# Kernel tuning notes

Measured on AMD Instinct MI355X. Metric: run time of the kernel, lower is better.

Reference implementation:

```python
import jax, jax.numpy as jnp
import numpy as np

B, N, D_MODEL = 8, 1024, 512
H, DK = 8, 64
STATIONS = 128
MASK_NEG = -1e9
LN_EPS = 1e-6


def setup_inputs() -> dict:
    key = jax.random.key(0)
    ks = jax.random.split(key, 9)
    return {
        "hidden_states": jax.random.normal(ks[0], (B, N, D_MODEL), dtype=jnp.float32),
        "rpe": jax.random.normal(ks[1], (B, H, N, N), dtype=jnp.float32) * 0.1,
        "Wq": jax.random.normal(ks[2], (H * DK, D_MODEL), dtype=jnp.float32) * 0.02,
        "Wk": jax.random.normal(ks[3], (H * DK, D_MODEL), dtype=jnp.float32) * 0.02,
        "Wv": jax.random.normal(ks[4], (H * DK, D_MODEL), dtype=jnp.float32) * 0.02,
        "fc_w": jax.random.normal(ks[5], (D_MODEL, H * DK), dtype=jnp.float32) * 0.02,
        "fc_b": jnp.zeros((D_MODEL,), dtype=jnp.float32),
        "ln_g": jnp.ones((D_MODEL,), dtype=jnp.float32),
        "ln_b": jnp.zeros((D_MODEL,), dtype=jnp.float32),
    }


def _star_mask(n, stations):
    # q_k_mask: query i attends to key j iff j < stations or i == j
    idx = jnp.arange(n)
    return (idx[None, :] < stations) | (idx[:, None] == idx[None, :])  # [n, n] bool


def reference(hidden_states, rpe, Wq, Wk, Wv, fc_w, fc_b, ln_g, ln_b):
    b, n, _ = hidden_states.shape
    residual = hidden_states
    q = (hidden_states @ Wq.T).reshape(b, n, H, DK)
    k = (hidden_states @ Wk.T).reshape(b, n, H, DK)
    v = (hidden_states @ Wv.T).reshape(b, n, H, DK)
    # sparse star+self-loop QK^T with inline RPE add (dense emulation of QKP_mm_tvm)
    scores = jnp.einsum("bihd,bjhd->bhij", q, k) + rpe  # [b,h,n,n]
    mask = _star_mask(n, STATIONS)
    scores = jnp.where(mask[None, None], scores, MASK_NEG)
    scores = scores / jnp.sqrt(jnp.float32(DK))
    attn = jax.nn.softmax(scores, axis=-1)
    # AttnV_mm_tvm: sparse attn-weights times V
    ctx = jnp.einsum("bhij,bjhd->bihd", attn, v).reshape(b, n, H * DK)
    ctx = ctx @ fc_w.T + fc_b + residual
    mu = jnp.mean(ctx, axis=-1, keepdims=True)
    var = jnp.var(ctx, axis=-1, keepdims=True)
    return (ctx - mu) / jnp.sqrt(var + LN_EPS) * ln_g + ln_b
```

## Files before the change

### kernel.cpp

```cpp
#include <hip/hip_runtime.h>
#include <hip/hip_bf16.h>
#include <math.h>

#define B_  8
#define N_  1024
#define DM  512
#define H_  8
#define DK_ 64
#define ST  128
#define QT  32

typedef __attribute__((ext_vector_type(8))) short short8;
typedef __attribute__((ext_vector_type(4))) float floatx4;

#define GLD16(gp, lp)                                                          \
    __builtin_amdgcn_global_load_lds(                                          \
        (const __attribute__((address_space(1))) void*)(gp),                   \
        (__attribute__((address_space(3))) void*)(lp), 16, 0, 0)

struct CastArgs {
    const float* src[5];
    unsigned short* dst[5];
    int n[5];
};

__global__ __launch_bounds__(256)
void cast_bf16_kernel(CastArgs a)
{
    const int j = blockIdx.y;
    const float* __restrict__ s = a.src[j];
    unsigned short* __restrict__ d = a.dst[j];
    const int n = a.n[j];
    int i = (blockIdx.x * 256 + threadIdx.x) * 8;
    if (i >= n) return;
    float4 x0 = *(const float4*)&s[i];
    float4 x1 = *(const float4*)&s[i + 4];
    ushort4 o0, o1;
    __hip_bfloat16 t;
    t = __float2bfloat16(x0.x); o0.x = *(unsigned short*)&t;
    t = __float2bfloat16(x0.y); o0.y = *(unsigned short*)&t;
    t = __float2bfloat16(x0.z); o0.z = *(unsigned short*)&t;
    t = __float2bfloat16(x0.w); o0.w = *(unsigned short*)&t;
    t = __float2bfloat16(x1.x); o1.x = *(unsigned short*)&t;
    t = __float2bfloat16(x1.y); o1.y = *(unsigned short*)&t;
    t = __float2bfloat16(x1.z); o1.z = *(unsigned short*)&t;
    t = __float2bfloat16(x1.w); o1.w = *(unsigned short*)&t;
    *(ushort4*)&d[i] = o0;
    *(ushort4*)&d[i + 4] = o1;
}

__device__ __forceinline__
void gemm_core(const unsigned short* __restrict__ A,
               const unsigned short* __restrict__ W,
               int m0, int n0, unsigned short* As, unsigned short* Bs,
               floatx4 acc[4][4])
{
    const int tid = threadIdx.x;
    const int lane = tid & 63;
    const int wave = tid >> 6;
    const int wm = wave >> 1, wn = wave & 1;
    const int srow = tid >> 2;
    const int skq  = (tid & 3) * 8;
    const unsigned short* Ag = A + (size_t)(m0 + srow) * 512 + skq;
    const unsigned short* Bg = W + (size_t)(n0 + srow) * 512 + skq;
    const int mrow = lane & 15;
    const int koff = (lane >> 4) * 8;

    for (int kt = 0; kt < 512; kt += 32) {
        __syncthreads();
        GLD16(Ag + kt,            &As[tid * 8]);
        GLD16(Ag + 64 * 512 + kt, &As[2048 + tid * 8]);
        GLD16(Bg + kt,            &Bs[tid * 8]);
        GLD16(Bg + 64 * 512 + kt, &Bs[2048 + tid * 8]);
        __syncthreads();
        short8 af[4], bf[4];
        #pragma unroll
        for (int t = 0; t < 4; ++t) {
            af[t] = *(const short8*)&As[(wm * 64 + t * 16 + mrow) * 32 + koff];
            bf[t] = *(const short8*)&Bs[(wn * 64 + t * 16 + mrow) * 32 + koff];
        }
        #pragma unroll
        for (int mt = 0; mt < 4; ++mt)
            #pragma unroll
            for (int nt = 0; nt < 4; ++nt)
                acc[mt][nt] = __builtin_amdgcn_mfma_f32_16x16x32_bf16(
                    af[mt], bf[nt], acc[mt][nt], 0, 0, 0);
    }
}

__global__ __launch_bounds__(256)
void qkv_gemm_kernel(const unsigned short* __restrict__ A,
                     const unsigned short* __restrict__ W0,
                     const unsigned short* __restrict__ W1,
                     const unsigned short* __restrict__ W2,
                     float* __restrict__ q, float* __restrict__ k,
                     float* __restrict__ v)
{
    __shared__ __align__(16) unsigned short As[128 * 32];
    __shared__ __align__(16) unsigned short Bs[128 * 32];
    const int by = blockIdx.y;
    const unsigned short* W = (by < 4) ? W0 : (by < 8 ? W1 : W2);
    float* C = (by < 4) ? q : (by < 8 ? k : v);
    const int m0 = blockIdx.x * 128;
    const int n0 = (by & 3) * 128;

    floatx4 acc[4][4];
    #pragma unroll
    for (int i = 0; i < 4; ++i)
        #pragma unroll
        for (int j = 0; j < 4; ++j)
            acc[i][j] = (floatx4){0.f, 0.f, 0.f, 0.f};

    gemm_core(A, W, m0, n0, As, Bs, acc);

    const int lane = threadIdx.x & 63;
    const int wave = threadIdx.x >> 6;
    const int wm = wave >> 1, wn = wave & 1;
    const int col = n0 + wn * 64 + (lane & 15);
    const int rq  = (lane >> 4) * 4;
    #pragma unroll
    for (int mt = 0; mt < 4; ++mt)
        #pragma unroll
        for (int nt = 0; nt < 4; ++nt)
            #pragma unroll
            for (int r = 0; r < 4; ++r)
                C[(size_t)(m0 + wm * 64 + mt * 16 + rq + r) * 512 + col + nt * 16]
                    = acc[mt][nt][r];
}

__global__ __launch_bounds__(256)
void fc_gemm_kernel(const unsigned short* __restrict__ A,
                    const unsigned short* __restrict__ W,
                    const float* __restrict__ bias,
                    const float* __restrict__ resid,
                    float* __restrict__ C)
{
    __shared__ __align__(16) unsigned short As[128 * 32];
    __shared__ __align__(16) unsigned short Bs[128 * 32];
    const int m0 = blockIdx.x * 128;
    const int n0 = blockIdx.y * 128;

    floatx4 acc[4][4];
    #pragma unroll
    for (int i = 0; i < 4; ++i)
        #pragma unroll
        for (int j = 0; j < 4; ++j)
            acc[i][j] = (floatx4){0.f, 0.f, 0.f, 0.f};

    gemm_core(A, W, m0, n0, As, Bs, acc);

    const int lane = threadIdx.x & 63;
    const int wave = threadIdx.x >> 6;
    const int wm = wave >> 1, wn = wave & 1;
    const int col = n0 + wn * 64 + (lane & 15);
    const int rq  = (lane >> 4) * 4;
    #pragma unroll
    for (int mt = 0; mt < 4; ++mt)
        #pragma unroll
        for (int nt = 0; nt < 4; ++nt) {
            const int c = col + nt * 16;
            const float b = bias[c];
            #pragma unroll
            for (int r = 0; r < 4; ++r) {
                const size_t row = (size_t)(m0 + wm * 64 + mt * 16 + rq + r);
                C[row * 512 + c] = acc[mt][nt][r] + b + resid[row * 512 + c];
            }
        }
}

__global__ __launch_bounds__(256)
void attn_kernel(const float* __restrict__ q, const float* __restrict__ k,
                 const float* __restrict__ v, const float* __restrict__ rpe,
                 unsigned short* __restrict__ ctx)
{
    __shared__ __align__(16) float Qs[64][34];
    __shared__ __align__(16) float KV[128 * 68];
    __shared__ __align__(16) float Ps[128][34];
    __shared__ float selfS[QT];

    const int tid = threadIdx.x;
    const int tx = tid & 15, ty = tid >> 4;
    const int qb = blockIdx.x * QT;
    const int h  = blockIdx.y;
    const int b  = blockIdx.z;

    const float* qg = q + (size_t)(b * N_ + qb) * DM + h * DK_;
    const float* kg = k + (size_t)b * N_ * DM + h * DK_;
    const float* vg = v + (size_t)b * N_ * DM + h * DK_;

    {
        const int row = tid >> 3;
        const int kc  = (tid & 7) << 3;
        float4 a  = *(const float4*)(qg + (size_t)row * DM + kc);
        float4 bq = *(const float4*)(qg + (size_t)row * DM + kc + 4);
        Qs[kc + 0][row] = a.x;  Qs[kc + 1][row] = a.y;
        Qs[kc + 2][row] = a.z;  Qs[kc + 3][row] = a.w;
        Qs[kc + 4][row] = bq.x; Qs[kc + 5][row] = bq.y;
        Qs[kc + 6][row] = bq.z; Qs[kc + 7][row] = bq.w;
    }
    #pragma unroll
    for (int it = 0; it < 8; ++it) {
        int id = tid + it * 256;
        int j  = id >> 4;
        int dc = (id & 15) << 2;
        float4 a = *(const float4*)(kg + (size_t)j * DM + dc);
        KV[(dc + 0) * 132 + j] = a.x;
        KV[(dc + 1) * 132 + j] = a.y;
        KV[(dc + 2) * 132 + j] = a.z;
        KV[(dc + 3) * 132 + j] = a.w;
    }
    __syncthreads();

    if (tid < QT) {
        int i = qb + tid;
        float sv = -1e30f;
        if (i >= ST) {
            float dot = 0.f;
            const float* krow = kg + (size_t)i * DM;
            for (int d = 0; d < DK_; ++d)
                dot = fmaf(Qs[d][tid], krow[d], dot);
            sv = (dot + rpe[((size_t)(b * H_ + h) * N_ + i) * N_ + i]) * 0.125f;
        }
        selfS[tid] = sv;
    }

    float s[2][8] = {};
    #pragma unroll 4
    for (int d = 0; d < 64; ++d) {
        float2 qv = *(const float2*)&Qs[d][ty << 1];
        float4 ka = *(const float4*)&KV[d * 132 + (tx << 3)];
        float4 kb = *(const float4*)&KV[d * 132 + (tx << 3) + 4];
        float kk_[8] = {ka.x, ka.y, ka.z, ka.w, kb.x, kb.y, kb.z, kb.w};
        #pragma unroll
        for (int c = 0; c < 8; ++c) {
            s[0][c] = fmaf(qv.x, kk_[c], s[0][c]);
            s[1][c] = fmaf(qv.y, kk_[c], s[1][c]);
        }
    }
    __syncthreads();

    float l_r[2], ps_r[2];
    #pragma unroll
    for (int r = 0; r < 2; ++r) {
        int i = qb + (ty << 1) + r;
        const float* rrow = rpe + ((size_t)(b * H_ + h) * N_ + i) * N_ + (tx << 3);
        float4 ra = *(const float4*)rrow;
        float4 rb = *(const float4*)(rrow + 4);
        float rr[8] = {ra.x, ra.y, ra.z, ra.w, rb.x, rb.y, rb.z, rb.w};
        float mx = -1e30f;
        #pragma unroll
        for (int c = 0; c < 8; ++c) {
            s[r][c] = (s[r][c] + rr[c]) * 0.125f;
            mx = fmaxf(mx, s[r][c]);
        }
        #pragma unroll
        for (int o = 1; o < 16; o <<= 1)
            mx = fmaxf(mx, __shfl_xor(mx, o, 64));
        float sm = selfS[(ty << 1) + r];
        mx = fmaxf(mx, sm);
        float ls = 0.f;
        float p[8];
        #pragma unroll
        for (int c = 0; c < 8; ++c) {
            p[c] = __expf(s[r][c] - mx);
            ls += p[c];
        }
        #pragma unroll
        for (int o = 1; o < 16; o <<= 1)
            ls += __shfl_xor(ls, o, 64);
        float pself = __expf(sm - mx);
        ls += pself;
        l_r[r] = ls; ps_r[r] = pself;
        #pragma unroll
        for (int c = 0; c < 8; ++c)
            Ps[(tx << 3) + c][(ty << 1) + r] = p[c];
    }
    __syncthreads();

    #pragma unroll
    for (int it = 0; it < 8; ++it) {
        int id = tid + it * 256;
        int j  = id >> 4;
        int dc = (id & 15) << 2;
        float4 a = *(const float4*)(vg + (size_t)j * DM + dc);
        *(float4*)&KV[j * 68 + dc] = a;
    }
    __syncthreads();

    float c2[2][4] = {};
    #pragma unroll 4
    for (int j = 0; j < 128; ++j) {
        float2 pv = *(const float2*)&Ps[j][ty << 1];
        float4 vv = *(const float4*)&KV[j * 68 + (tx << 2)];
        float vv_[4] = {vv.x, vv.y, vv.z, vv.w};
        #pragma unroll
        for (int c = 0; c < 4; ++c) {
            c2[0][c] = fmaf(pv.x, vv_[c], c2[0][c]);
            c2[1][c] = fmaf(pv.y, vv_[c], c2[1][c]);
        }
    }
    #pragma unroll
    for (int r = 0; r < 2; ++r) {
        int qr = (ty << 1) + r;
        int i  = qb + qr;
        if (i >= ST) {
            float4 sv4 = *(const float4*)(vg + (size_t)i * DM + (tx << 2));
            float pself = ps_r[r];
            c2[r][0] = fmaf(pself, sv4.x, c2[r][0]);
            c2[r][1] = fmaf(pself, sv4.y, c2[r][1]);
            c2[r][2] = fmaf(pself, sv4.z, c2[r][2]);
            c2[r][3] = fmaf(pself, sv4.w, c2[r][3]);
        }
        float inv = 1.0f / l_r[r];
        ushort4 o;
        __hip_bfloat16 t;
        t = __float2bfloat16(c2[r][0] * inv); o.x = *(unsigned short*)&t;
        t = __float2bfloat16(c2[r][1] * inv); o.y = *(unsigned short*)&t;
        t = __float2bfloat16(c2[r][2] * inv); o.z = *(unsigned short*)&t;
        t = __float2bfloat16(c2[r][3] * inv); o.w = *(unsigned short*)&t;
        *(ushort4*)&ctx[(size_t)(b * N_ + i) * DM + h * DK_ + (tx << 2)] = o;
    }
}

__global__ __launch_bounds__(256)
void ln_kernel(float* __restrict__ io, const float* __restrict__ g,
               const float* __restrict__ bb)
{
    const int t = blockIdx.x;
    const int tid = threadIdx.x;
    float* row = io + (size_t)t * DM;
    float2 x = *(const float2*)&row[tid * 2];
    float s  = x.x + x.y;
    float ss = fmaf(x.x, x.x, x.y * x.y);
    #pragma unroll
    for (int o = 1; o < 64; o <<= 1) {
        s  += __shfl_xor(s,  o, 64);
        ss += __shfl_xor(ss, o, 64);
    }
    __shared__ float wsum[4], wsq[4];
    const int w = tid >> 6;
    if ((tid & 63) == 0) { wsum[w] = s; wsq[w] = ss; }
    __syncthreads();
    s  = wsum[0] + wsum[1] + wsum[2] + wsum[3];
    ss = wsq[0]  + wsq[1]  + wsq[2]  + wsq[3];
    const float mean = s * (1.0f / DM);
    const float var  = ss * (1.0f / DM) - mean * mean;
    const float rstd = rsqrtf(var + 1e-6f);
    float2 gg = *(const float2*)&g[tid * 2];
    float2 bv = *(const float2*)&bb[tid * 2];
    x.x = (x.x - mean) * rstd * gg.x + bv.x;
    x.y = (x.y - mean) * rstd * gg.y + bv.y;
    *(float2*)&row[tid * 2] = x;
}

extern "C" void kernel_launch(void* const* d_in, const int* in_sizes, int n_in,
                              void* d_out, int out_size, void* d_ws, size_t ws_size,
                              hipStream_t stream)
{
    (void)in_sizes; (void)n_in; (void)out_size; (void)ws_size;
    const float* hidden = (const float*)d_in[0];
    const float* rpe    = (const float*)d_in[1];
    const float* Wq     = (const float*)d_in[2];
    const float* Wk     = (const float*)d_in[3];
    const float* Wv     = (const float*)d_in[4];
    const float* fc_w   = (const float*)d_in[5];
    const float* fc_b   = (const float*)d_in[6];
    const float* ln_g   = (const float*)d_in[7];
    const float* ln_b   = (const float*)d_in[8];
    float* out = (float*)d_out;
    char* ws = (char*)d_ws;

    const size_t MB = 1024 * 1024;
    float*          qb = (float*)(ws + 0 * MB);
    float*          kb = (float*)(ws + 16 * MB);
    float*          vb = (float*)(ws + 32 * MB);
    unsigned short* hb = (unsigned short*)(ws + 48 * MB);
    unsigned short* cb = (unsigned short*)(ws + 56 * MB);
    unsigned short* wq = (unsigned short*)(ws + 64 * MB);
    unsigned short* wk = (unsigned short*)(ws + 64 * MB + 512 * 1024);
    unsigned short* wv = (unsigned short*)(ws + 65 * MB);
    unsigned short* wf = (unsigned short*)(ws + 65 * MB + 512 * 1024);

    CastArgs ca;
    ca.src[0] = hidden; ca.dst[0] = hb; ca.n[0] = B_ * N_ * DM;
    ca.src[1] = Wq;     ca.dst[1] = wq; ca.n[1] = DM * DM;
    ca.src[2] = Wk;     ca.dst[2] = wk; ca.n[2] = DM * DM;
    ca.src[3] = Wv;     ca.dst[3] = wv; ca.n[3] = DM * DM;
    ca.src[4] = fc_w;   ca.dst[4] = wf; ca.n[4] = DM * DM;
    cast_bf16_kernel<<<dim3(2048, 5), 256, 0, stream>>>(ca);

    qkv_gemm_kernel<<<dim3(64, 12), 256, 0, stream>>>(hb, wq, wk, wv, qb, kb, vb);
    attn_kernel<<<dim3(N_ / QT, H_, B_), 256, 0, stream>>>(qb, kb, vb, rpe, cb);
    fc_gemm_kernel<<<dim3(64, 4), 256, 0, stream>>>(cb, wf, fc_b, hidden, out);
    ln_kernel<<<B_ * N_, 256, 0, stream>>>(out, ln_g, ln_b);
}
```

Measured before the change: 426.5 us.

## Store Q/K/V as bf16 head-major and run attention with MFMA

The QKV GEMM now writes bf16 Q and K in [b,h,n,d] layout and V transposed as [b,h,d,n], replacing fp32 row-major buffers. The attention kernel is rewritten to process 64 queries per block, computing QK^T against the 128 station keys and P·V with bf16 MFMA instructions instead of scalar FMA loops through LDS. This cuts intermediate memory traffic and scalar compute. In exchange, the softmax probabilities are rounded to bf16 and the QKV epilogue uses scattered stores for the transposed layout.

```diff
diff --git a/kernel.cpp b/kernel.cpp
--- a/kernel.cpp
+++ b/kernel.cpp
@@ -8,7 +8,6 @@
 #define H_  8
 #define DK_ 64
 #define ST  128
-#define QT  32
 
 typedef __attribute__((ext_vector_type(8))) short short8;
 typedef __attribute__((ext_vector_type(4))) float floatx4;
@@ -17,6 +16,16 @@
     __builtin_amdgcn_global_load_lds(                                          \
         (const __attribute__((address_space(1))) void*)(gp),                   \
         (__attribute__((address_space(3))) void*)(lp), 16, 0, 0)
+
+__device__ __forceinline__ float b2f(short u) {
+    union { unsigned int i; float f; } c;
+    c.i = ((unsigned int)(unsigned short)u) << 16;
+    return c.f;
+}
+__device__ __forceinline__ unsigned short f2b(float f) {
+    __hip_bfloat16 t = __float2bfloat16(f);
+    return *(unsigned short*)&t;
+}
 
 struct CastArgs {
     const float* src[5];
@@ -36,15 +45,8 @@
     float4 x0 = *(const float4*)&s[i];
     float4 x1 = *(const float4*)&s[i + 4];
     ushort4 o0, o1;
-    __hip_bfloat16 t;
-    t = __float2bfloat16(x0.x); o0.x = *(unsigned short*)&t;
-    t = __float2bfloat16(x0.y); o0.y = *(unsigned short*)&t;
-    t = __float2bfloat16(x0.z); o0.z = *(unsigned short*)&t;
-    t = __float2bfloat16(x0.w); o0.w = *(unsigned short*)&t;
-    t = __float2bfloat16(x1.x); o1.x = *(unsigned short*)&t;
-    t = __float2bfloat16(x1.y); o1.y = *(unsigned short*)&t;
-    t = __float2bfloat16(x1.z); o1.z = *(unsigned short*)&t;
-    t = __float2bfloat16(x1.w); o1.w = *(unsigned short*)&t;
+    o0.x = f2b(x0.x); o0.y = f2b(x0.y); o0.z = f2b(x0.z); o0.w = f2b(x0.w);
+    o1.x = f2b(x1.x); o1.y = f2b(x1.y); o1.z = f2b(x1.z); o1.w = f2b(x1.w);
     *(ushort4*)&d[i] = o0;
     *(ushort4*)&d[i + 4] = o1;
 }
@@ -93,14 +95,15 @@
                      const unsigned short* __restrict__ W0,
                      const unsigned short* __restrict__ W1,
                      const unsigned short* __restrict__ W2,
-                     float* __restrict__ q, float* __restrict__ k,
-                     float* __restrict__ v)
+                     unsigned short* __restrict__ qo,
+                     unsigned short* __restrict__ ko,
+                     unsigned short* __restrict__ vto)
 {
     __shared__ __align__(16) unsigned short As[128 * 32];
     __shared__ __align__(16) unsigned short Bs[128 * 32];
     const int by = blockIdx.y;
-    const unsigned short* W = (by < 4) ? W0 : (by < 8 ? W1 : W2);
-    float* C = (by < 4) ? q : (by < 8 ? k : v);
+    const int sel = by >> 2;
+    const unsigned short* W = (sel == 0) ? W0 : (sel == 1 ? W1 : W2);
     const int m0 = blockIdx.x * 128;
     const int n0 = (by & 3) * 128;
 
@@ -116,16 +119,42 @@
     const int lane = threadIdx.x & 63;
     const int wave = threadIdx.x >> 6;
     const int wm = wave >> 1, wn = wave & 1;
-    const int col = n0 + wn * 64 + (lane & 15);
-    const int rq  = (lane >> 4) * 4;
-    #pragma unroll
-    for (int mt = 0; mt < 4; ++mt)
-        #pragma unroll
-        for (int nt = 0; nt < 4; ++nt)
+    const int lx = lane & 15;
+    const int rq = (lane >> 4) * 4;
+
+    if (sel == 2) {
+        #pragma unroll
+        for (int mt = 0; mt < 4; ++mt) {
+            const int mrow = m0 + wm * 64 + mt * 16 + rq;
+            const int bb = mrow >> 10, tok = mrow & 1023;
             #pragma unroll
-            for (int r = 0; r < 4; ++r)
-                C[(size_t)(m0 + wm * 64 + mt * 16 + rq + r) * 512 + col + nt * 16]
-                    = acc[mt][nt][r];
+            for (int nt = 0; nt < 4; ++nt) {
+                const int c = n0 + wn * 64 + nt * 16 + lx;
+                const int hh = c >> 6, d = c & 63;
+                ushort4 pk;
+                pk.x = f2b(acc[mt][nt][0]); pk.y = f2b(acc[mt][nt][1]);
+                pk.z = f2b(acc[mt][nt][2]); pk.w = f2b(acc[mt][nt][3]);
+                *(ushort4*)&vto[((size_t)(bb * H_ + hh) * DK_ + d) * N_ + tok] = pk;
+            }
+        }
+    } else {
+        unsigned short* O = (sel == 0) ? qo : ko;
+        #pragma unroll
+        for (int mt = 0; mt < 4; ++mt) {
+            const int mrow = m0 + wm * 64 + mt * 16 + rq;
+            const int bb = mrow >> 10, tok = mrow & 1023;
+            #pragma unroll
+            for (int nt = 0; nt < 4; ++nt) {
+                const int c = n0 + wn * 64 + nt * 16 + lx;
+                const int hh = c >> 6, d = c & 63;
+                unsigned short* p =
+                    O + ((size_t)(bb * H_ + hh) * N_ + tok) * DK_ + d;
+                #pragma unroll
+                for (int r = 0; r < 4; ++r)
+                    p[(size_t)r * DK_] = f2b(acc[mt][nt][r]);
+            }
+        }
+    }
 }
 
 __global__ __launch_bounds__(256)
@@ -169,156 +198,141 @@
 }
 
 __global__ __launch_bounds__(256)
-void attn_kernel(const float* __restrict__ q, const float* __restrict__ k,
-                 const float* __restrict__ v, const float* __restrict__ rpe,
+void attn_kernel(const unsigned short* __restrict__ qg,
+                 const unsigned short* __restrict__ kg,
+                 const unsigned short* __restrict__ vtg,
+                 const float* __restrict__ rpe,
                  unsigned short* __restrict__ ctx)
 {
-    __shared__ __align__(16) float Qs[64][34];
-    __shared__ __align__(16) float KV[128 * 68];
-    __shared__ __align__(16) float Ps[128][34];
-    __shared__ float selfS[QT];
-
-    const int tid = threadIdx.x;
-    const int tx = tid & 15, ty = tid >> 4;
-    const int qb = blockIdx.x * QT;
-    const int h  = blockIdx.y;
-    const int b  = blockIdx.z;
-
-    const float* qg = q + (size_t)(b * N_ + qb) * DM + h * DK_;
-    const float* kg = k + (size_t)b * N_ * DM + h * DK_;
-    const float* vg = v + (size_t)b * N_ * DM + h * DK_;
-
+    __shared__ __align__(16) unsigned short P[64 * 136];
+
+    const int tid  = threadIdx.x;
+    const int lane = tid & 63;
+    const int w    = tid >> 6;
+    const int lx   = lane & 15;
+    const int quad = lane >> 4;
+    const int qb = blockIdx.x * 64;
+    const int h  = blockIdx.y, b = blockIdx.z;
+    const int bh = b * H_ + h;
+    const unsigned short* qh  = qg  + (size_t)bh * N_ * DK_;
+    const unsigned short* kh  = kg  + (size_t)bh * N_ * DK_;
+    const unsigned short* vth = vtg + (size_t)bh * DK_ * N_;
+    const float* rp = rpe + ((size_t)bh * N_ + qb) * N_;
+    const bool has_self = (qb >= ST);
+
+    float sself = -1e30f;
+    if (has_self) {
+        const int i = qb + w * 16 + lx;
+        const unsigned short* qr = qh + (size_t)i * DK_ + quad * 16;
+        const unsigned short* kr = kh + (size_t)i * DK_ + quad * 16;
+        short8 q0 = *(const short8*)qr, q1 = *(const short8*)(qr + 8);
+        short8 k0 = *(const short8*)kr, k1 = *(const short8*)(kr + 8);
+        float dot = 0.f;
+        #pragma unroll
+        for (int j = 0; j < 8; ++j) {
+            dot = fmaf(b2f(q0[j]), b2f(k0[j]), dot);
+            dot = fmaf(b2f(q1[j]), b2f(k1[j]), dot);
+        }
+        dot += __shfl_xor(dot, 16, 64);
+        dot += __shfl_xor(dot, 32, 64);
+        const float rd = rp[(size_t)(w * 16 + lx) * N_ + (qb + w * 16 + lx)];
+        sself = (dot + rd) * 0.125f;
+    }
+
+    float rv[4][8];
     {
-        const int row = tid >> 3;
-        const int kc  = (tid & 7) << 3;
-        float4 a  = *(const float4*)(qg + (size_t)row * DM + kc);
-        float4 bq = *(const float4*)(qg + (size_t)row * DM + kc + 4);
-        Qs[kc + 0][row] = a.x;  Qs[kc + 1][row] = a.y;
-        Qs[kc + 2][row] = a.z;  Qs[kc + 3][row] = a.w;
-        Qs[kc + 4][row] = bq.x; Qs[kc + 5][row] = bq.y;
-        Qs[kc + 6][row] = bq.z; Qs[kc + 7][row] = bq.w;
-    }
-    #pragma unroll
-    for (int it = 0; it < 8; ++it) {
-        int id = tid + it * 256;
-        int j  = id >> 4;
-        int dc = (id & 15) << 2;
-        float4 a = *(const float4*)(kg + (size_t)j * DM + dc);
-        KV[(dc + 0) * 132 + j] = a.x;
-        KV[(dc + 1) * 132 + j] = a.y;
-        KV[(dc + 2) * 132 + j] = a.z;
-        KV[(dc + 3) * 132 + j] = a.w;
-    }
-    __syncthreads();
-
-    if (tid < QT) {
-        int i = qb + tid;
-        float sv = -1e30f;
-        if (i >= ST) {
-            float dot = 0.f;
-            const float* krow = kg + (size_t)i * DM;
-            for (int d = 0; d < DK_; ++d)
-                dot = fmaf(Qs[d][tid], krow[d], dot);
-            sv = (dot + rpe[((size_t)(b * H_ + h) * N_ + i) * N_ + i]) * 0.125f;
-        }
-        selfS[tid] = sv;
-    }
-
-    float s[2][8] = {};
-    #pragma unroll 4
-    for (int d = 0; d < 64; ++d) {
-        float2 qv = *(const float2*)&Qs[d][ty << 1];
-        float4 ka = *(const float4*)&KV[d * 132 + (tx << 3)];
-        float4 kb = *(const float4*)&KV[d * 132 + (tx << 3) + 4];
-        float kk_[8] = {ka.x, ka.y, ka.z, ka.w, kb.x, kb.y, kb.z, kb.w};
-        #pragma unroll
-        for (int c = 0; c < 8; ++c) {
-            s[0][c] = fmaf(qv.x, kk_[c], s[0][c]);
-            s[1][c] = fmaf(qv.y, kk_[c], s[1][c]);
-        }
-    }
-    __syncthreads();
-
-    float l_r[2], ps_r[2];
-    #pragma unroll
-    for (int r = 0; r < 2; ++r) {
-        int i = qb + (ty << 1) + r;
-        const float* rrow = rpe + ((size_t)(b * H_ + h) * N_ + i) * N_ + (tx << 3);
-        float4 ra = *(const float4*)rrow;
-        float4 rb = *(const float4*)(rrow + 4);
-        float rr[8] = {ra.x, ra.y, ra.z, ra.w, rb.x, rb.y, rb.z, rb.w};
+        const float* rbase = rp + (size_t)(w * 16 + quad * 4) * N_ + lx;
+        #pragma unroll
+        for (int r = 0; r < 4; ++r)
+            #pragma unroll
+            for (int nt = 0; nt < 8; ++nt)
+                rv[r][nt] = rbase[(size_t)r * N_ + nt * 16];
+    }
+
+    short8 aq[2];
+    {
+        const unsigned short* qrow =
+            qh + (size_t)(qb + w * 16 + lx) * DK_ + quad * 8;
+        aq[0] = *(const short8*)qrow;
+        aq[1] = *(const short8*)(qrow + 32);
+    }
+    floatx4 sacc[8];
+    #pragma unroll
+    for (int nt = 0; nt < 8; ++nt) sacc[nt] = (floatx4){0.f, 0.f, 0.f, 0.f};
+    #pragma unroll
+    for (int nt = 0; nt < 8; ++nt) {
+        const unsigned short* krow =
+            kh + (size_t)(nt * 16 + lx) * DK_ + quad * 8;
+        short8 b0 = *(const short8*)krow;
+        short8 b1 = *(const short8*)(krow + 32);
+        sacc[nt] = __builtin_amdgcn_mfma_f32_16x16x32_bf16(aq[0], b0, sacc[nt], 0, 0, 0);
+        sacc[nt] = __builtin_amdgcn_mfma_f32_16x16x32_bf16(aq[1], b1, sacc[nt], 0, 0, 0);
+    }
+
+    float l4[4], ps4[4];
+    #pragma unroll
+    for (int r = 0; r < 4; ++r) {
+        float sv[8];
         float mx = -1e30f;
         #pragma unroll
-        for (int c = 0; c < 8; ++c) {
-            s[r][c] = (s[r][c] + rr[c]) * 0.125f;
-            mx = fmaxf(mx, s[r][c]);
+        for (int nt = 0; nt < 8; ++nt) {
+            sv[nt] = (sacc[nt][r] + rv[r][nt]) * 0.125f;
+            mx = fmaxf(mx, sv[nt]);
         }
         #pragma unroll
         for (int o = 1; o < 16; o <<= 1)
             mx = fmaxf(mx, __shfl_xor(mx, o, 64));
-        float sm = selfS[(ty << 1) + r];
-        mx = fmaxf(mx, sm);
-        float ls = 0.f;
-        float p[8];
-        #pragma unroll
-        for (int c = 0; c < 8; ++c) {
-            p[c] = __expf(s[r][c] - mx);
-            ls += p[c];
+        const float ss = __shfl(sself, quad * 4 + r, 64);
+        mx = fmaxf(mx, ss);
+        float sum = 0.f;
+        #pragma unroll
+        for (int nt = 0; nt < 8; ++nt) {
+            sv[nt] = __expf(sv[nt] - mx);
+            sum += sv[nt];
         }
         #pragma unroll
         for (int o = 1; o < 16; o <<= 1)
-            ls += __shfl_xor(ls, o, 64);
-        float pself = __expf(sm - mx);
-        ls += pself;
-        l_r[r] = ls; ps_r[r] = pself;
-        #pragma unroll
-        for (int c = 0; c < 8; ++c)
-            Ps[(tx << 3) + c][(ty << 1) + r] = p[c];
+            sum += __shfl_xor(sum, o, 64);
+        const float ps = has_self ? __expf(ss - mx) : 0.f;
+        l4[r] = sum + ps;
+        ps4[r] = ps;
+        const int row = w * 16 + quad * 4 + r;
+        #pragma unroll
+        for (int nt = 0; nt < 8; ++nt)
+            P[row * 136 + nt * 16 + lx] = f2b(sv[nt]);
     }
     __syncthreads();
 
-    #pragma unroll
-    for (int it = 0; it < 8; ++it) {
-        int id = tid + it * 256;
-        int j  = id >> 4;
-        int dc = (id & 15) << 2;
-        float4 a = *(const float4*)(vg + (size_t)j * DM + dc);
-        *(float4*)&KV[j * 68 + dc] = a;
-    }
-    __syncthreads();
-
-    float c2[2][4] = {};
-    #pragma unroll 4
-    for (int j = 0; j < 128; ++j) {
-        float2 pv = *(const float2*)&Ps[j][ty << 1];
-        float4 vv = *(const float4*)&KV[j * 68 + (tx << 2)];
-        float vv_[4] = {vv.x, vv.y, vv.z, vv.w};
-        #pragma unroll
-        for (int c = 0; c < 4; ++c) {
-            c2[0][c] = fmaf(pv.x, vv_[c], c2[0][c]);
-            c2[1][c] = fmaf(pv.y, vv_[c], c2[1][c]);
-        }
-    }
-    #pragma unroll
-    for (int r = 0; r < 2; ++r) {
-        int qr = (ty << 1) + r;
-        int i  = qb + qr;
-        if (i >= ST) {
-            float4 sv4 = *(const float4*)(vg + (size_t)i * DM + (tx << 2));
-            float pself = ps_r[r];
-            c2[r][0] = fmaf(pself, sv4.x, c2[r][0]);
-            c2[r][1] = fmaf(pself, sv4.y, c2[r][1]);
-            c2[r][2] = fmaf(pself, sv4.z, c2[r][2]);
-            c2[r][3] = fmaf(pself, sv4.w, c2[r][3]);
-        }
-        float inv = 1.0f / l_r[r];
-        ushort4 o;
-        __hip_bfloat16 t;
-        t = __float2bfloat16(c2[r][0] * inv); o.x = *(unsigned short*)&t;
-        t = __float2bfloat16(c2[r][1] * inv); o.y = *(unsigned short*)&t;
-        t = __float2bfloat16(c2[r][2] * inv); o.z = *(unsigned short*)&t;
-        t = __float2bfloat16(c2[r][3] * inv); o.w = *(unsigned short*)&t;
-        *(ushort4*)&ctx[(size_t)(b * N_ + i) * DM + h * DK_ + (tx << 2)] = o;
+    short8 ap[4];
+    #pragma unroll
+    for (int ks = 0; ks < 4; ++ks)
+        ap[ks] = *(const short8*)&P[(w * 16 + lx) * 136 + ks * 32 + quad * 8];
+    floatx4 oacc[4];
+    #pragma unroll
+    for (int nt = 0; nt < 4; ++nt) oacc[nt] = (floatx4){0.f, 0.f, 0.f, 0.f};
+    #pragma unroll
+    for (int nt = 0; nt < 4; ++nt) {
+        const unsigned short* vrow = vth + (size_t)(nt * 16 + lx) * N_;
+        #pragma unroll
+        for (int ks = 0; ks < 4; ++ks) {
+            short8 bv = *(const short8*)(vrow + ks * 32 + quad * 8);
+            oacc[nt] = __builtin_amdgcn_mfma_f32_16x16x32_bf16(ap[ks], bv, oacc[nt], 0, 0, 0);
+        }
+    }
+
+    #pragma unroll
+    for (int r = 0; r < 4; ++r) {
+        const int i = qb + w * 16 + quad * 4 + r;
+        const float inv = 1.0f / l4[r];
+        const float ps = ps4[r];
+        #pragma unroll
+        for (int nt = 0; nt < 4; ++nt) {
+            const int d = nt * 16 + lx;
+            float o = oacc[nt][r];
+            if (has_self)
+                o = fmaf(ps, b2f((short)vth[(size_t)d * N_ + i]), o);
+            ctx[((size_t)(b * N_) + i) * DM + h * DK_ + d] = f2b(o * inv);
+        }
     }
 }
 
@@ -371,15 +385,15 @@
     char* ws = (char*)d_ws;
 
     const size_t MB = 1024 * 1024;
-    float*          qb = (float*)(ws + 0 * MB);
-    float*          kb = (float*)(ws + 16 * MB);
-    float*          vb = (float*)(ws + 32 * MB);
-    unsigned short* hb = (unsigned short*)(ws + 48 * MB);
-    unsigned short* cb = (unsigned short*)(ws + 56 * MB);
-    unsigned short* wq = (unsigned short*)(ws + 64 * MB);
-    unsigned short* wk = (unsigned short*)(ws + 64 * MB + 512 * 1024);
-    unsigned short* wv = (unsigned short*)(ws + 65 * MB);
-    unsigned short* wf = (unsigned short*)(ws + 65 * MB + 512 * 1024);
+    unsigned short* hb  = (unsigned short*)(ws + 0 * MB);
+    unsigned short* wq  = (unsigned short*)(ws + 8 * MB);
+    unsigned short* wk  = (unsigned short*)(ws + 8 * MB + 512 * 1024);
+    unsigned short* wv  = (unsigned short*)(ws + 9 * MB);
+    unsigned short* wf  = (unsigned short*)(ws + 9 * MB + 512 * 1024);
+    unsigned short* qB  = (unsigned short*)(ws + 16 * MB);
+    unsigned short* kB  = (unsigned short*)(ws + 24 * MB);
+    unsigned short* vtB = (unsigned short*)(ws + 32 * MB);
+    unsigned short* cb  = (unsigned short*)(ws + 40 * MB);
 
     CastArgs ca;
     ca.src[0] = hidden; ca.dst[0] = hb; ca.n[0] = B_ * N_ * DM;
@@ -389,8 +403,8 @@
     ca.src[4] = fc_w;   ca.dst[4] = wf; ca.n[4] = DM * DM;
     cast_bf16_kernel<<<dim3(2048, 5), 256, 0, stream>>>(ca);
 
-    qkv_gemm_kernel<<<dim3(64, 12), 256, 0, stream>>>(hb, wq, wk, wv, qb, kb, vb);
-    attn_kernel<<<dim3(N_ / QT, H_, B_), 256, 0, stream>>>(qb, kb, vb, rpe, cb);
+    qkv_gemm_kernel<<<dim3(64, 12), 256, 0, stream>>>(hb, wq, wk, wv, qB, kB, vtB);
+    attn_kernel<<<dim3(16, H_, B_), 256, 0, stream>>>(qB, kB, vtB, rpe, cb);
     fc_gemm_kernel<<<dim3(64, 4), 256, 0, stream>>>(cb, wf, fc_b, hidden, out);
     ln_kernel<<<B_ * N_, 256, 0, stream>>>(out, ln_g, ln_b);
 }
```

Measured after the change: 400.2 us. -6.2%, faster.
